# Optimization experiments

Measured on AMD Instinct MI355X. Metric: run time of the kernel, lower is better.

## Reference

```python
import jax, jax.numpy as jnp
import numpy as np

N, D, C = 8192, 512, 1000


def setup_inputs() -> dict:
    key = jax.random.key(0)
    k1, k2, k3 = jax.random.split(key, 3)
    features = jax.random.normal(k1, (N, D), dtype=jnp.float32)
    centers = jax.random.normal(k2, (C, D), dtype=jnp.float32)
    labels = jax.random.randint(k3, (N,), 0, C, dtype=jnp.int64)
    return {"features": features, "centers": centers, "labels": labels}


def _l2_normalize(x, axis=1, eps=1e-12):
    # matches torch F.normalize(p=2): x / max(||x||, eps)
    norm = jnp.sqrt(jnp.sum(x * x, axis=axis, keepdims=True))
    return x / jnp.maximum(norm, eps)


def reference(features, centers, labels):
    f = _l2_normalize(features, axis=1)          # [N, D]
    c = _l2_normalize(centers, axis=1)           # [C, D]
    centers_batch = c[labels]                    # [N, D]
    pos_distances = 1.0 - jnp.sum(f * centers_batch, axis=1)      # [N]
    neg_distances = 1.0 - jnp.matmul(f, f.T)                       # [N, N]
    losses = pos_distances[:, None] - neg_distances                # [N, N]
    diff_class = labels[:, None] != labels[None, :]                # [N, N]
    valid = diff_class & (losses > 0.0)                            # [N, N]
    losses = jnp.where(valid, losses, 0.0)
    num_valid_pairs = jnp.sum(valid, axis=1)                       # [N]
    num_valid_pairs = jnp.where(num_valid_pairs > 0, num_valid_pairs, 1)
    sample_losses = jnp.sum(losses, axis=1) / num_valid_pairs.astype(losses.dtype)
    num_valid_samples = jnp.sum(sample_losses > 0.0)
    loss = jnp.sum(sample_losses)
    loss = jnp.where(num_valid_samples > 0,
                     loss / num_valid_samples.astype(loss.dtype), loss)
    return loss
```

## Files before the change

### kernel.cpp

```cpp
#include <hip/hip_runtime.h>
#include <hip/hip_bf16.h>
#include <hip/hip_fp8.h>
#include <stdint.h>
#include <math.h>

#define N_ROWS 8192
#define DIM    512
#define BM     128
#define BK     64
#define NB     (N_ROWS / BM)
#define NTRI   (NB * (NB + 1) / 2)
#define NKT    (DIM / BK)

typedef float f32x4 __attribute__((ext_vector_type(4)));

__global__ __launch_bounds__(256) void k_prep(const float* __restrict__ feats,
                                              const float* __restrict__ centers,
                                              const int* __restrict__ labels,
                                              unsigned char* __restrict__ f_q,
                                              float* __restrict__ posdot,
                                              float* __restrict__ Ssum,
                                              int* __restrict__ Kcnt) {
    const int row = blockIdx.x;
    const int t = threadIdx.x;
    const float* src = feats + (size_t)row * DIM;
    float v0 = src[t], v1 = src[t + 256];
    float ss = v0 * v0 + v1 * v1;
#pragma unroll
    for (int m = 1; m < 64; m <<= 1) ss += __shfl_xor(ss, m, 64);
    __shared__ float red[12];
    const int lane = t & 63, wid = t >> 6;
    if (lane == 0) red[wid] = ss;
    __syncthreads();
    const float tot = red[0] + red[1] + red[2] + red[3];
    const float scale = 1.0f / fmaxf(sqrtf(tot), 1e-12f);
    const float n0 = v0 * scale, n1 = v1 * scale;
    {
        __hip_fp8_e4m3 q0(n0), q1(n1);
        f_q[(size_t)row * DIM + t]       = *reinterpret_cast<const unsigned char*>(&q0);
        f_q[(size_t)row * DIM + t + 256] = *reinterpret_cast<const unsigned char*>(&q1);
    }

    const int lab = labels[row];
    const float* c = centers + (size_t)lab * DIM;
    const float c0 = c[t], c1 = c[t + 256];
    float cc = c0 * c0 + c1 * c1;
    float d  = n0 * c0 + n1 * c1;
#pragma unroll
    for (int m = 1; m < 64; m <<= 1) {
        cc += __shfl_xor(cc, m, 64);
        d  += __shfl_xor(d, m, 64);
    }
    if (lane == 0) { red[4 + wid] = cc; red[8 + wid] = d; }
    __syncthreads();
    if (t == 0) {
        const float ctot = red[4] + red[5] + red[6] + red[7];
        const float dtot = red[8] + red[9] + red[10] + red[11];
        posdot[row] = dtot / fmaxf(sqrtf(ctot), 1e-12f);
        Ssum[row] = 0.0f;
        Kcnt[row] = 0;
    }
}

__global__ __launch_bounds__(256) void k_pair(const unsigned char* __restrict__ f_q,
                                              const int* __restrict__ labels,
                                              const float* __restrict__ pd,
                                              float* __restrict__ Ssum,
                                              int* __restrict__ Kcnt) {
    __shared__ __align__(16) unsigned char sA[2][BM * BK];
    __shared__ __align__(16) unsigned char sB[2][BM * BK];
    __shared__ int   s_lr[BM];
    __shared__ int   s_lc[BM];
    __shared__ float s_pd[BM];
    __shared__ float s_pc[BM];

    const int tid  = threadIdx.x;
    const int lane = tid & 63;
    const int wid  = tid >> 6;
    const int wr   = wid >> 1, wc = wid & 1;

    const int t = blockIdx.x;
    int bi = (int)floor((2.0 * NB + 1.0 - sqrt((2.0 * NB + 1.0) * (2.0 * NB + 1.0) - 8.0 * (double)t)) * 0.5);
    while (bi * NB - bi * (bi - 1) / 2 > t) --bi;
    while ((bi + 1) * NB - (bi + 1) * bi / 2 <= t) ++bi;
    const int bj = bi + (t - (bi * NB - bi * (bi - 1) / 2));
    const int rowBase = bi * BM;
    const int colBase = bj * BM;
    const bool offdiag = (bi != bj);

    if (tid < BM) {
        s_lr[tid] = labels[rowBase + tid];
        s_pd[tid] = pd[rowBase + tid];
    } else {
        s_lc[tid - BM] = labels[colBase + tid - BM];
        s_pc[tid - BM] = pd[colBase + tid - BM];
    }

    f32x4 acc[4][4] = {};

    const int srow  = lane >> 2;
    const int sc16  = (lane & 3) ^ ((lane >> 3) & 3);

#define STAGE(KT, P)                                                                       \
    do {                                                                                   \
        const int k0_ = (KT) * BK;                                                         \
        _Pragma("unroll")                                                                  \
        for (int i_ = 0; i_ < 2; ++i_) {                                                   \
            const int ch_ = wid * 2 + i_;                                                  \
            const int r_  = ch_ * 16 + srow;                                               \
            const unsigned char* gA_ = f_q + ((size_t)(rowBase + r_) * DIM + k0_ + sc16 * 16); \
            const unsigned char* gB_ = f_q + ((size_t)(colBase + r_) * DIM + k0_ + sc16 * 16); \
            __builtin_amdgcn_global_load_lds(                                              \
                (const __attribute__((address_space(1))) void*)gA_,                        \
                (__attribute__((address_space(3))) void*)(&sA[P][ch_ * 1024]), 16, 0, 0);  \
            __builtin_amdgcn_global_load_lds(                                              \
                (const __attribute__((address_space(1))) void*)gB_,                        \
                (__attribute__((address_space(3))) void*)(&sB[P][ch_ * 1024]), 16, 0, 0);  \
        }                                                                                  \
    } while (0)

#define COMPUTE(P)                                                                         \
    do {                                                                                   \
        _Pragma("unroll")                                                                  \
        for (int kk = 0; kk < 2; ++kk) {                                                   \
            long aF[4], bF[4];                                                             \
            const int c8 = kk * 4 + (lane >> 4);                                           \
            _Pragma("unroll")                                                              \
            for (int m = 0; m < 4; ++m) {                                                  \
                const int r = wr * 64 + m * 16 + (lane & 15);                              \
                const int c16p = (c8 >> 1) ^ ((r >> 1) & 3);                               \
                aF[m] = *(const long*)(&sA[P][r * 64 + c16p * 16 + (c8 & 1) * 8]);         \
            }                                                                              \
            _Pragma("unroll")                                                              \
            for (int n = 0; n < 4; ++n) {                                                  \
                const int r = wc * 64 + n * 16 + (lane & 15);                              \
                const int c16p = (c8 >> 1) ^ ((r >> 1) & 3);                               \
                bF[n] = *(const long*)(&sB[P][r * 64 + c16p * 16 + (c8 & 1) * 8]);         \
            }                                                                              \
            _Pragma("unroll")                                                              \
            for (int m = 0; m < 4; ++m)                                                    \
                _Pragma("unroll")                                                          \
                for (int n = 0; n < 4; ++n)                                                \
                    acc[m][n] = __builtin_amdgcn_mfma_f32_16x16x32_fp8_fp8(aF[m], bF[n], acc[m][n], 0, 0, 0); \
        }                                                                                  \
    } while (0)

    STAGE(0, 0);
    __syncthreads();

    for (int kt = 0; kt < NKT - 1; ++kt) {
        const int cur = kt & 1;
        STAGE(kt + 1, cur ^ 1);
        COMPUTE(cur);
        __syncthreads();
    }
    COMPUTE((NKT - 1) & 1);

#undef STAGE
#undef COMPUTE

    float colS[4] = {0.f, 0.f, 0.f, 0.f};
    int   colK[4] = {0, 0, 0, 0};
    int   lcv[4]; float pcv[4];
#pragma unroll
    for (int n = 0; n < 4; ++n) {
        const int jl = wc * 64 + n * 16 + (lane & 15);
        lcv[n] = s_lc[jl];
        pcv[n] = s_pc[jl];
    }

#pragma unroll
    for (int m = 0; m < 4; ++m) {
        float rowS[4] = {0.f, 0.f, 0.f, 0.f};
        int   rowK[4] = {0, 0, 0, 0};
        const int rbase = wr * 64 + m * 16 + ((lane >> 4) << 2);
        int myLr[4]; float myPd[4];
#pragma unroll
        for (int g = 0; g < 4; ++g) { myLr[g] = s_lr[rbase + g]; myPd[g] = s_pd[rbase + g]; }
#pragma unroll
        for (int n = 0; n < 4; ++n) {
#pragma unroll
            for (int g = 0; g < 4; ++g) {
                const float s = acc[m][n][g];
                const bool diff = (myLr[g] != lcv[n]);
                if (diff && s > myPd[g]) { rowS[g] += (s - myPd[g]); rowK[g] += 1; }
                if (offdiag && diff && s > pcv[n]) { colS[n] += (s - pcv[n]); colK[n] += 1; }
            }
        }
#pragma unroll
        for (int g = 0; g < 4; ++g) {
#pragma unroll
            for (int d = 1; d < 16; d <<= 1) {
                rowS[g] += __shfl_xor(rowS[g], d, 64);
                rowK[g] += __shfl_xor(rowK[g], d, 64);
            }
        }
        if ((lane & 15) == 0) {
#pragma unroll
            for (int g = 0; g < 4; ++g) {
                const int r = rowBase + rbase + g;
                atomicAdd(&Ssum[r], rowS[g]);
                atomicAdd(&Kcnt[r], rowK[g]);
            }
        }
    }

    if (offdiag) {
#pragma unroll
        for (int n = 0; n < 4; ++n) {
#pragma unroll
            for (int d = 16; d < 64; d <<= 1) {
                colS[n] += __shfl_xor(colS[n], d, 64);
                colK[n] += __shfl_xor(colK[n], d, 64);
            }
        }
        if (lane < 16) {
#pragma unroll
            for (int n = 0; n < 4; ++n) {
                const int c = colBase + wc * 64 + n * 16 + lane;
                atomicAdd(&Ssum[c], colS[n]);
                atomicAdd(&Kcnt[c], colK[n]);
            }
        }
    }
}

__global__ __launch_bounds__(1024) void k_final(const float* __restrict__ Ssum,
                                                const int* __restrict__ Kcnt,
                                                float* __restrict__ out) {
    const int t = threadIdx.x;
    double sum = 0.0; int cnt = 0;
    for (int i = t; i < N_ROWS; i += 1024) {
        const int k = Kcnt[i];
        if (k > 0) { sum += (double)Ssum[i] / (double)k; cnt += 1; }
    }
#pragma unroll
    for (int d = 1; d < 64; d <<= 1) {
        sum += __shfl_xor(sum, d, 64);
        cnt += __shfl_xor(cnt, d, 64);
    }
    __shared__ double s_sum[16];
    __shared__ int    s_cnt[16];
    const int lane = t & 63, wid = t >> 6;
    if (lane == 0) { s_sum[wid] = sum; s_cnt[wid] = cnt; }
    __syncthreads();
    if (t == 0) {
        double ts = 0.0; int tc = 0;
#pragma unroll
        for (int w = 0; w < 16; ++w) { ts += s_sum[w]; tc += s_cnt[w]; }
        out[0] = (float)(tc > 0 ? ts / (double)tc : ts);
    }
}

extern "C" void kernel_launch(void* const* d_in, const int* in_sizes, int n_in,
                              void* d_out, int out_size, void* d_ws, size_t ws_size,
                              hipStream_t stream) {
    const float* features = (const float*)d_in[0];
    const float* centers  = (const float*)d_in[1];
    const int*   labels   = (const int*)d_in[2];
    float* out = (float*)d_out;

    char* ws = (char*)d_ws;
    unsigned char* f_q    = (unsigned char*)(ws);
    float*         posdot = (float*)(ws + 0x400000);
    float*         Ssum   = (float*)(ws + 0x400000 + 0x8000);
    int*           Kcnt   = (int*)  (ws + 0x400000 + 0x10000);

    k_prep<<<N_ROWS, 256, 0, stream>>>(features, centers, labels, f_q, posdot, Ssum, Kcnt);
    k_pair<<<NTRI, 256, 0, stream>>>(f_q, labels, posdot, Ssum, Kcnt);
    k_final<<<1, 1024, 0, stream>>>(Ssum, Kcnt, out);
}
```

Baseline: 90.09 us.

## Permute fp8 feature layout for 128-bit LDS fragment loads and triple-buffer K pipeline

The prep kernel now writes each quantized feature row in a permuted byte order. Each lane's two MFMA k-slices then sit contiguously, so COMPUTE fetches them with a single 16-byte LDS read instead of two 8-byte reads. The pair kernel also moves from double to triple buffering, keeping two stages of global-to-LDS loads in flight. It uses explicit vmcnt waits and raw s_barrier calls in place of __syncthreads. In exchange it uses more LDS, which may reduce occupancy, and it depends on hand-written waitcnt correctness.

```diff
diff --git a/kernel.cpp b/kernel.cpp
--- a/kernel.cpp
+++ b/kernel.cpp
@@ -13,6 +13,8 @@
 #define NKT    (DIM / BK)
 
 typedef float f32x4 __attribute__((ext_vector_type(4)));
+typedef long  lng2  __attribute__((ext_vector_type(2)));
+
 
 __global__ __launch_bounds__(256) void k_prep(const float* __restrict__ feats,
                                               const float* __restrict__ centers,
@@ -37,8 +39,17 @@
     const float n0 = v0 * scale, n1 = v1 * scale;
     {
         __hip_fp8_e4m3 q0(n0), q1(n1);
-        f_q[(size_t)row * DIM + t]       = *reinterpret_cast<const unsigned char*>(&q0);
-        f_q[(size_t)row * DIM + t + 256] = *reinterpret_cast<const unsigned char*>(&q1);
+#pragma unroll
+        for (int j = 0; j < 2; ++j) {
+            const int k  = t + j * 256;
+            const int kt = k >> 6, k6 = k & 63;
+            const int h  = (k6 >> 5) & 1;
+            const int u  = (k6 >> 3) & 3;
+            const int pos = kt * 64 + u * 16 + h * 8 + (k6 & 7);
+            const unsigned char qb = (j == 0) ? *reinterpret_cast<const unsigned char*>(&q0)
+                                              : *reinterpret_cast<const unsigned char*>(&q1);
+            f_q[(size_t)row * DIM + pos] = qb;
+        }
     }
 
     const int lab = labels[row];
@@ -67,8 +78,8 @@
                                               const float* __restrict__ pd,
                                               float* __restrict__ Ssum,
                                               int* __restrict__ Kcnt) {
-    __shared__ __align__(16) unsigned char sA[2][BM * BK];
-    __shared__ __align__(16) unsigned char sB[2][BM * BK];
+    __shared__ __align__(16) unsigned char sA[3][BM * BK];
+    __shared__ __align__(16) unsigned char sB[3][BM * BK];
     __shared__ int   s_lr[BM];
     __shared__ int   s_lc[BM];
     __shared__ float s_pd[BM];
@@ -98,8 +109,8 @@
 
     f32x4 acc[4][4] = {};
 
-    const int srow  = lane >> 2;
-    const int sc16  = (lane & 3) ^ ((lane >> 3) & 3);
+    const int srow = lane >> 2;
+    const int slu  = (lane & 3) ^ ((lane >> 3) & 3);
 
 #define STAGE(KT, P)                                                                       \
     do {                                                                                   \
@@ -108,8 +119,8 @@
         for (int i_ = 0; i_ < 2; ++i_) {                                                   \
             const int ch_ = wid * 2 + i_;                                                  \
             const int r_  = ch_ * 16 + srow;                                               \
-            const unsigned char* gA_ = f_q + ((size_t)(rowBase + r_) * DIM + k0_ + sc16 * 16); \
-            const unsigned char* gB_ = f_q + ((size_t)(colBase + r_) * DIM + k0_ + sc16 * 16); \
+            const unsigned char* gA_ = f_q + ((size_t)(rowBase + r_) * DIM + k0_ + slu * 16); \
+            const unsigned char* gB_ = f_q + ((size_t)(colBase + r_) * DIM + k0_ + slu * 16); \
             __builtin_amdgcn_global_load_lds(                                              \
                 (const __attribute__((address_space(1))) void*)gA_,                        \
                 (__attribute__((address_space(3))) void*)(&sA[P][ch_ * 1024]), 16, 0, 0);  \
@@ -119,42 +130,50 @@
         }                                                                                  \
     } while (0)
 
+    const int pu = (lane >> 4) ^ ((lane >> 1) & 3);
+
 #define COMPUTE(P)                                                                         \
     do {                                                                                   \
-        _Pragma("unroll")                                                                  \
-        for (int kk = 0; kk < 2; ++kk) {                                                   \
-            long aF[4], bF[4];                                                             \
-            const int c8 = kk * 4 + (lane >> 4);                                           \
-            _Pragma("unroll")                                                              \
-            for (int m = 0; m < 4; ++m) {                                                  \
-                const int r = wr * 64 + m * 16 + (lane & 15);                              \
-                const int c16p = (c8 >> 1) ^ ((r >> 1) & 3);                               \
-                aF[m] = *(const long*)(&sA[P][r * 64 + c16p * 16 + (c8 & 1) * 8]);         \
-            }                                                                              \
+        lng2 aF[4], bF[4];                                                                 \
+        _Pragma("unroll")                                                                  \
+        for (int m = 0; m < 4; ++m) {                                                      \
+            const int r = wr * 64 + m * 16 + (lane & 15);                                  \
+            aF[m] = *(const lng2*)(&sA[P][r * 64 + pu * 16]);                              \
+        }                                                                                  \
+        _Pragma("unroll")                                                                  \
+        for (int n = 0; n < 4; ++n) {                                                      \
+            const int r = wc * 64 + n * 16 + (lane & 15);                                  \
+            bF[n] = *(const lng2*)(&sB[P][r * 64 + pu * 16]);                              \
+        }                                                                                  \
+        _Pragma("unroll")                                                                  \
+        for (int m = 0; m < 4; ++m)                                                        \
             _Pragma("unroll")                                                              \
             for (int n = 0; n < 4; ++n) {                                                  \
-                const int r = wc * 64 + n * 16 + (lane & 15);                              \
-                const int c16p = (c8 >> 1) ^ ((r >> 1) & 3);                               \
-                bF[n] = *(const long*)(&sB[P][r * 64 + c16p * 16 + (c8 & 1) * 8]);         \
+                acc[m][n] = __builtin_amdgcn_mfma_f32_16x16x32_fp8_fp8(aF[m].x, bF[n].x, acc[m][n], 0, 0, 0); \
+                acc[m][n] = __builtin_amdgcn_mfma_f32_16x16x32_fp8_fp8(aF[m].y, bF[n].y, acc[m][n], 0, 0, 0); \
             }                                                                              \
-            _Pragma("unroll")                                                              \
-            for (int m = 0; m < 4; ++m)                                                    \
-                _Pragma("unroll")                                                          \
-                for (int n = 0; n < 4; ++n)                                                \
-                    acc[m][n] = __builtin_amdgcn_mfma_f32_16x16x32_fp8_fp8(aF[m], bF[n], acc[m][n], 0, 0, 0); \
-        }                                                                                  \
     } while (0)
 
     STAGE(0, 0);
-    __syncthreads();
-
-    for (int kt = 0; kt < NKT - 1; ++kt) {
-        const int cur = kt & 1;
-        STAGE(kt + 1, cur ^ 1);
-        COMPUTE(cur);
-        __syncthreads();
-    }
-    COMPUTE((NKT - 1) & 1);
+    STAGE(1, 1);
+    asm volatile("s_waitcnt lgkmcnt(0)" ::: "memory");
+    asm volatile("s_waitcnt vmcnt(4)" ::: "memory");
+    __builtin_amdgcn_s_barrier();
+    __builtin_amdgcn_sched_barrier(0);
+
+    {
+        int p0 = 0, p1 = 1, p2 = 2;
+#pragma unroll
+        for (int kt = 0; kt < NKT - 1; ++kt) {
+            STAGE((kt + 2) & (NKT - 1), p2);
+            COMPUTE(p0);
+            asm volatile("s_waitcnt vmcnt(4)" ::: "memory");
+            __builtin_amdgcn_s_barrier();
+            __builtin_amdgcn_sched_barrier(0);
+            const int tmp = p0; p0 = p1; p1 = p2; p2 = tmp;
+        }
+        COMPUTE(p0);
+    }
 
 #undef STAGE
 #undef COMPUTE
```

Measured after the change: 93.60 us. 1.04x slower.
